# Kernel tuning notes

Hardware: AMD Instinct MI355X
Metric: run time of the kernel (lower is better)

Reference implementation:

```python
import jax, jax.numpy as jnp
import numpy as np

SAMPLING = 16   # VGG16 feature stride
POOL = 7        # adaptive max pool output size
KMAX = 5        # max bin window; valid for ROI feature extents <= 28 cells
NEG = jnp.float32(-1e30)


def _bin_bounds(s0, L, i):
    # torch AdaptiveMaxPool2d bin i over a length-L crop starting at s0:
    # [s0 + floor(i*L/P), s0 + ceil((i+1)*L/P))
    bs = s0 + (i * L) // POOL
    be = s0 + ((i + 1) * L + POOL - 1) // POOL
    return bs, be


def setup_inputs() -> dict:
    key = jax.random.key(0)
    ks = jax.random.split(key, 12)
    N, C, Hf, Wf = 1024, 512, 50, 84
    Himg, Wimg = Hf * SAMPLING, Wf * SAMPLING
    # post-ReLU VGG features -> non-negative
    featmap = jax.random.uniform(ks[0], (1, C, Hf, Wf), dtype=jnp.float32)
    # ROI boxes [x0, y0, x1, y1] in pixel coords, extents in [32, 448] px
    x0 = jax.random.randint(ks[1], (N,), 0, Wimg - 448)
    y0 = jax.random.randint(ks[2], (N,), 0, Himg - 448)
    w = jax.random.randint(ks[3], (N,), 32, 449)
    h = jax.random.randint(ks[4], (N,), 32, 449)
    roi = jnp.stack([x0, y0, x0 + w, y0 + h], axis=1).astype(jnp.int32)
    d = C * POOL * POOL  # 25088
    W1 = jax.random.normal(ks[5], (d, 4096), dtype=jnp.float32) * 0.01
    b1 = jnp.zeros((4096,), jnp.float32)
    W2 = jax.random.normal(ks[6], (4096, 4096), dtype=jnp.float32) * 0.01
    b2 = jnp.zeros((4096,), jnp.float32)
    Wc = jax.random.normal(ks[7], (4096, 3), dtype=jnp.float32) * 0.01
    bc = jnp.zeros((3,), jnp.float32)
    Wr = jax.random.normal(ks[8], (4096, 12), dtype=jnp.float32) * 0.01
    br = jnp.zeros((12,), jnp.float32)
    return {"featmap": featmap, "roi": roi, "W1": W1, "b1": b1, "W2": W2,
            "b2": b2, "Wc": Wc, "bc": bc, "Wr": Wr, "br": br}


def _roipool(featmap, roi):
    fm = featmap[0]                       # (C, Hf, Wf)
    C, Hf, Wf = fm.shape
    rf = roi // SAMPLING                  # floor, coords are non-negative
    x0, y0, x1, y1 = rf[:, 0], rf[:, 1], rf[:, 2], rf[:, 3]
    # width expand: if x1-x0 <= 1 -> grow right if in-bounds else grow left
    nw = (x1 - x0) <= 1
    x0n = jnp.where(nw & ~(x1 < Wf), x0 - 1, x0)
    x1n = jnp.where(nw & (x1 < Wf), x1 + 1, x1)
    nh = (y1 - y0) <= 1
    y0n = jnp.where(nh & ~(y1 < Hf), y0 - 1, y0)
    y1n = jnp.where(nh & (y1 < Hf), y1 + 1, y1)
    # python slice semantics clamp to array bounds
    xs, xe = jnp.clip(x0n, 0, Wf), jnp.clip(x1n, 0, Wf)
    ys, ye = jnp.clip(y0n, 0, Hf), jnp.clip(y1n, 0, Hf)
    Lx, Ly = xe - xs, ye - ys
    ar = jnp.arange(KMAX)
    rows = []
    for i in range(POOL):                 # fixed 7x7 bins
        hs, he = _bin_bounds(ys, Ly, i)
        h_idx = hs[:, None] + ar          # (N, K)
        h_ok = h_idx < he[:, None]
        h_idx = jnp.clip(h_idx, 0, Hf - 1)
        cols = []
        for j in range(POOL):
            ws_, we_ = _bin_bounds(xs, Lx, j)
            w_idx = ws_[:, None] + ar     # (N, K)
            w_ok = w_idx < we_[:, None]
            w_idx = jnp.clip(w_idx, 0, Wf - 1)
            patch = fm[:, h_idx[:, :, None], w_idx[:, None, :]]  # (C, N, K, K)
            m = h_ok[:, :, None] & w_ok[:, None, :]              # (N, K, K)
            patch = jnp.where(m[None], patch, NEG)
            cols.append(patch.max(axis=(2, 3)))                  # (C, N)
        rows.append(jnp.stack(cols, 0))   # (7, C, N)
    pool = jnp.stack(rows, 0)             # (7, 7, C, N)
    return pool.transpose(3, 2, 0, 1).reshape(roi.shape[0], -1)  # (N, C*49)


def reference(featmap, roi, W1, b1, W2, b2, Wc, bc, Wr, br):
    pooled = _roipool(featmap, roi)       # (N, 25088)
    h = (pooled @ W1 + b1) @ W2 + b2      # two Linears, no activation (as in source)
    output_cls = jax.nn.softmax(h @ Wc + bc, axis=1)
    output_reg = h @ Wr + br
    return output_cls, output_reg
```

## Files before the change

kernel.cpp:

```cpp
#include <hip/hip_runtime.h>
#include <hip/hip_bf16.h>
#include <cstdint>
#include <cstddef>

typedef __attribute__((ext_vector_type(4))) float f32x4;
typedef __attribute__((ext_vector_type(8))) short s16x8;
typedef __attribute__((ext_vector_type(4))) unsigned short u16x4;

__device__ __forceinline__ unsigned short f2bf(float f) {
    union { float f; unsigned u; } v; v.f = f;
    unsigned u = v.u;
    u += 0x7fffu + ((u >> 16) & 1u);
    return (unsigned short)(u >> 16);
}
__device__ __forceinline__ float lo_f(unsigned v) {
    union { unsigned u; float f; } w; w.u = v << 16; return w.f;
}
__device__ __forceinline__ float hi_f(unsigned v) {
    union { unsigned u; float f; } w; w.u = v & 0xffff0000u; return w.f;
}


__global__ __launch_bounds__(512) void prepA(
        const float* __restrict__ fm, unsigned short* __restrict__ fmT,
        const float* __restrict__ W2, const float* __restrict__ Wc,
        const float* __restrict__ Wr, float* __restrict__ partial1) {
    const int g5 = blockIdx.x / 5, r5 = blockIdx.x % 5;
    const int t = threadIdx.x;
    if (r5 < 4) {
        const int unit = g5 * 4 + r5;
        if (unit >= 1056) return;
        __shared__ float tile[2][32][33];
        const int sub = t >> 8, tt = t & 255;
        const int tid = unit * 2 + sub;
        const int p0 = (tid % 132) * 32, c0 = (tid / 132) * 32;
        const int tx = tt & 31, ty = tt >> 5;
        #pragma unroll
        for (int yy = ty; yy < 32; yy += 8) {
            int p = p0 + tx;
            if (p < 4200) tile[sub][yy][tx] = fm[(size_t)(c0 + yy) * 4200 + p];
        }
        __syncthreads();
        #pragma unroll
        for (int yy = ty; yy < 32; yy += 8) {
            int p = p0 + yy;
            if (p < 4200) fmT[(size_t)p * 512 + c0 + tx] = f2bf(tile[sub][tx][yy]);
        }
    } else {
        const int v = g5;
        if (v >= 256) return;
        const int bx = v & 31, ky = v >> 5;
        const int lane = t & 63, wave = t >> 6;
        const int r0 = bx * 128 + wave * 16;
        const int k0 = ky * 512;
        const int lr = lane & 15, lks = lane >> 4;
        const float* ap = W2 + (size_t)(r0 + lr) * 4096 + k0 + lks * 8;
        f32x4 acc = {0.f, 0.f, 0.f, 0.f};
        for (int s = 0; s < 16; ++s) {
            f32x4 f0 = *(const f32x4*)(ap + s * 32);
            f32x4 f1 = *(const f32x4*)(ap + s * 32 + 4);
            union { unsigned short us[8]; s16x8 v; } a, b;
            const int i0 = k0 + s * 32 + lks * 8;
            #pragma unroll
            for (int e = 0; e < 8; ++e) {
                int i = i0 + e;
                float bv = (lr < 3) ? Wc[i * 3 + lr] : (lr < 15) ? Wr[i * 12 + lr - 3] : 0.f;
                b.us[e] = f2bf(bv);
            }
            a.us[0] = f2bf(f0.x); a.us[1] = f2bf(f0.y);
            a.us[2] = f2bf(f0.z); a.us[3] = f2bf(f0.w);
            a.us[4] = f2bf(f1.x); a.us[5] = f2bf(f1.y);
            a.us[6] = f2bf(f1.z); a.us[7] = f2bf(f1.w);
            acc = __builtin_amdgcn_mfma_f32_16x16x32_bf16(a.v, b.v, acc, 0, 0, 0);
        }
        const int row = r0 + (lane >> 4) * 4;
        float* op = partial1 + ((size_t)ky * 4096 + row) * 16 + lr;
        #pragma unroll
        for (int q = 0; q < 4; ++q) op[q * 16] = acc[q];
    }
}

__global__ __launch_bounds__(256) void reduce_wf(
        const float* __restrict__ partial1, const float* __restrict__ b2,
        const float* __restrict__ Wc, const float* __restrict__ Wr,
        const float* __restrict__ bc, const float* __restrict__ br,
        float* __restrict__ Wf16, unsigned short* __restrict__ WfT,
        float* __restrict__ bfv) {
    const int t = threadIdx.x;
    if (blockIdx.x < 256) {
        int idx = blockIdx.x * 256 + t;
        float s = 0.f;
        #pragma unroll
        for (int sp = 0; sp < 8; ++sp) s += partial1[sp * 65536 + idx];
        Wf16[idx] = s;
        int i = idx >> 4, j = idx & 15;
        WfT[(size_t)j * 4096 + i] = f2bf(s);
    } else {
        float acc[15];
        #pragma unroll
        for (int j = 0; j < 15; ++j) acc[j] = 0.f;
        for (int i = t; i < 4096; i += 256) {
            float bv = b2[i];
            #pragma unroll
            for (int j = 0; j < 15; ++j)
                acc[j] += bv * ((j < 3) ? Wc[i * 3 + j] : Wr[i * 12 + (j - 3)]);
        }
        const int lane = t & 63, wv = t >> 6;
        __shared__ float red[4][15];
        #pragma unroll
        for (int j = 0; j < 15; ++j) {
            float x = acc[j];
            #pragma unroll
            for (int off = 32; off >= 1; off >>= 1) x += __shfl_xor(x, off, 64);
            if (lane == 0) red[wv][j] = x;
        }
        __syncthreads();
        if (t < 15)
            bfv[t] = red[0][t] + red[1][t] + red[2][t] + red[3][t]
                   + ((t < 3) ? bc[t] : br[t - 3]);
    }
}

#define PB(NH, NW) { \
    uint2 v[NH * NW]; \
    _Pragma("unroll") for (int r = 0; r < NH; ++r) \
        _Pragma("unroll") for (int s = 0; s < NW; ++s) \
            v[r * NW + s] = *(const uint2*)(base + ho[r] + wo[s]); \
    float a0 = lo_f(v[0].x), a1 = hi_f(v[0].x); \
    float a2 = lo_f(v[0].y), a3 = hi_f(v[0].y); \
    _Pragma("unroll") for (int q = 1; q < NH * NW; ++q) { \
        a0 = fmaxf(a0, lo_f(v[q].x)); a1 = fmaxf(a1, hi_f(v[q].x)); \
        a2 = fmaxf(a2, lo_f(v[q].y)); a3 = fmaxf(a3, hi_f(v[q].y)); } \
    m0 = a0; m1 = a1; m2 = a2; m3 = a3; } break;

__global__ __launch_bounds__(256) void megaB(
        const unsigned short* __restrict__ fmT, const int* __restrict__ roi,
        unsigned short* __restrict__ pooled,
        const float* __restrict__ W1, const unsigned short* __restrict__ WfT,
        float* __restrict__ partial2) {
    const int g4 = blockIdx.x >> 2, r4 = blockIdx.x & 3;
    const int t = threadIdx.x;
    if (r4 < 3) {
        const int sb = g4 * 3 + r4;
        if (sb >= 3136) return;
        const int bx = sb % 392, ky = sb / 392;
        const int lane = t & 63, wave = t >> 6;
        const int r0 = bx * 64 + wave * 16;
        const int k0 = ky * 512;
        const int lr = lane & 15, lks = lane >> 4;
        const float* ap = W1 + (size_t)(r0 + lr) * 4096 + k0 + lks * 8;
        const unsigned short* bp = WfT + (size_t)lr * 4096 + k0 + lks * 8;
        f32x4 acc = {0.f, 0.f, 0.f, 0.f};
        #pragma unroll 4
        for (int s = 0; s < 16; ++s) {
            f32x4 f0 = __builtin_nontemporal_load((const f32x4*)(ap + s * 32));
            f32x4 f1 = __builtin_nontemporal_load((const f32x4*)(ap + s * 32 + 4));
            s16x8 b = *(const s16x8*)(bp + s * 32);
            union { unsigned short us[8]; s16x8 v; } a;
            a.us[0] = f2bf(f0.x); a.us[1] = f2bf(f0.y);
            a.us[2] = f2bf(f0.z); a.us[3] = f2bf(f0.w);
            a.us[4] = f2bf(f1.x); a.us[5] = f2bf(f1.y);
            a.us[6] = f2bf(f1.z); a.us[7] = f2bf(f1.w);
            acc = __builtin_amdgcn_mfma_f32_16x16x32_bf16(a.v, b, acc, 0, 0, 0);
        }
        const int row = r0 + (lane >> 4) * 4;
        float* op = partial2 + ((size_t)ky * 25088 + row) * 16 + lr;
        #pragma unroll
        for (int q = 0; q < 4; ++q) __builtin_nontemporal_store(acc[q], op + q * 16);
    } else {
        const int n = g4;
        if (n >= 1024) return;
        __shared__ int hoff[7][5], woff[7][5], hcnt[7], wcnt[7];
        if (t == 0) {
            int x0 = roi[n*4+0] / 16, y0 = roi[n*4+1] / 16;
            int x1 = roi[n*4+2] / 16, y1 = roi[n*4+3] / 16;
            if (x1 - x0 <= 1) { if (x1 < 84) x1 += 1; else x0 -= 1; }
            if (y1 - y0 <= 1) { if (y1 < 50) y1 += 1; else y0 -= 1; }
            int xs = min(max(x0, 0), 84), xe = min(max(x1, 0), 84);
            int ys = min(max(y0, 0), 50), ye = min(max(y1, 0), 50);
            int Lx = xe - xs, Ly = ye - ys;
            #pragma unroll
            for (int i = 0; i < 7; ++i) {
                int b0 = ys + (i * Ly) / 7, b1 = ys + ((i + 1) * Ly + 6) / 7;
                hcnt[i] = min(b1, b0 + 5) - b0;
                int c0 = xs + (i * Lx) / 7, c1 = xs + ((i + 1) * Lx + 6) / 7;
                wcnt[i] = min(c1, c0 + 5) - c0;
                #pragma unroll
                for (int q = 0; q < 5; ++q) {
                    hoff[i][q] = (b0 + q) * 43008;
                    woff[i][q] = (c0 + q) * 512;
                }
            }
        }
        __syncthreads();
        const int g = t >> 7;
        const int c4 = (t & 127) * 4;
        const unsigned short* base = fmT + c4;
        unsigned short* orow = pooled + (size_t)n * 25088;
        for (int bp = 0; bp < 25; ++bp) {
            int bin = bp * 2 + g;
            if (bin < 49) {
                int bi = bin / 7, bj = bin - bi * 7;
                int ho[5], wo[5];
                #pragma unroll
                for (int q = 0; q < 5; ++q) { ho[q] = hoff[bi][q]; wo[q] = woff[bj][q]; }
                int nh = hcnt[bi], nw = wcnt[bj];
                float m0, m1, m2, m3;
                switch ((nh - 1) * 5 + (nw - 1)) {
                    case  0: PB(1,1)  case  1: PB(1,2)  case  2: PB(1,3)
                    case  3: PB(1,4)  case  4: PB(1,5)
                    case  5: PB(2,1)  case  6: PB(2,2)  case  7: PB(2,3)
                    case  8: PB(2,4)  case  9: PB(2,5)
                    case 10: PB(3,1)  case 11: PB(3,2)  case 12: PB(3,3)
                    case 13: PB(3,4)  case 14: PB(3,5)
                    case 15: PB(4,1)  case 16: PB(4,2)  case 17: PB(4,3)
                    case 18: PB(4,4)  case 19: PB(4,5)
                    case 20: PB(5,1)  case 21: PB(5,2)  case 22: PB(5,3)
                    case 23: PB(5,4)  case 24: PB(5,5)
                    default: m0 = m1 = m2 = m3 = 0.f; break;
                }
                u16x4 o;
                o.x = f2bf(m0); o.y = f2bf(m1); o.z = f2bf(m2); o.w = f2bf(m3);
                __builtin_nontemporal_store(o, (u16x4*)(orow + bin * 512 + c4));
            }
        }
    }
}

__global__ __launch_bounds__(256) void reduce_wbig(
        const float* __restrict__ partial2, const float* __restrict__ Wf16,
        const float* __restrict__ bfv, const float* __restrict__ b1,
        unsigned short* __restrict__ WbigT, float* __restrict__ bbig) {
    const int t = threadIdx.x;
    if (blockIdx.x < 98) {
        const int r = blockIdx.x * 256 + t;
        float sj[16];
        #pragma unroll
        for (int j = 0; j < 16; ++j) sj[j] = 0.f;
        #pragma unroll
        for (int sp = 0; sp < 8; ++sp) {
            const float4* pp = (const float4*)(partial2 + ((size_t)sp * 25088 + r) * 16);
            float4 a = pp[0], b = pp[1], c = pp[2], d = pp[3];
            sj[0] += a.x; sj[1] += a.y; sj[2]  += a.z; sj[3]  += a.w;
            sj[4] += b.x; sj[5] += b.y; sj[6]  += b.z; sj[7]  += b.w;
            sj[8] += c.x; sj[9] += c.y; sj[10] += c.z; sj[11] += c.w;
            sj[12] += d.x; sj[13] += d.y; sj[14] += d.z; sj[15] += d.w;
        }
        const int c = r / 49, bin = r - c * 49;
        const int p = bin * 512 + c;
        #pragma unroll
        for (int j = 0; j < 16; ++j)
            WbigT[(size_t)j * 25088 + p] = f2bf(sj[j]);
    } else {
        float acc[15];
        #pragma unroll
        for (int j = 0; j < 15; ++j) acc[j] = 0.f;
        for (int i = t; i < 4096; i += 256) {
            float bv = b1[i];
            #pragma unroll
            for (int j = 0; j < 15; ++j) acc[j] += bv * Wf16[i * 16 + j];
        }
        const int lane = t & 63, wv = t >> 6;
        __shared__ float red[4][15];
        #pragma unroll
        for (int j = 0; j < 15; ++j) {
            float x = acc[j];
            #pragma unroll
            for (int off = 32; off >= 1; off >>= 1) x += __shfl_xor(x, off, 64);
            if (lane == 0) red[wv][j] = x;
        }
        __syncthreads();
        if (t < 16) {
            float s = 0.f;
            if (t < 15)
                s = red[0][t] + red[1][t] + red[2][t] + red[3][t] + bfv[t];
            bbig[t] = s;
        }
    }
}

__global__ __launch_bounds__(256) void final_gemm(
        const unsigned short* __restrict__ pooled,
        const unsigned short* __restrict__ WbigT,
        float* __restrict__ partialG) {
    const int t = threadIdx.x, lane = t & 63, wave = t >> 6;
    const int m0 = blockIdx.x * 16, kz = blockIdx.y;
    const int lr = lane & 15, lks = lane >> 4;
    f32x4 acc = {0.f, 0.f, 0.f, 0.f};
    const unsigned short* arow = pooled + (size_t)(m0 + lr) * 25088 + kz * 3136 + lks * 8;
    const unsigned short* brow = WbigT + (size_t)lr * 25088 + kz * 3136 + lks * 8;
    for (int s = wave; s < 98; s += 4) {
        s16x8 a = __builtin_nontemporal_load((const s16x8*)(arow + s * 32));
        s16x8 b = *(const s16x8*)(brow + s * 32);
        acc = __builtin_amdgcn_mfma_f32_16x16x32_bf16(a, b, acc, 0, 0, 0);
    }
    __shared__ float red[4][64][4];
    #pragma unroll
    for (int r = 0; r < 4; ++r) red[wave][lane][r] = acc[r];
    __syncthreads();
    if (wave == 0) {
        #pragma unroll
        for (int r = 0; r < 4; ++r) {
            float s = red[0][lane][r] + red[1][lane][r] + red[2][lane][r] + red[3][lane][r];
            int row = m0 + (lane >> 4) * 4 + r;
            partialG[((size_t)kz * 1024 + row) * 16 + (lane & 15)] = s;
        }
    }
}

__global__ __launch_bounds__(256) void finalize_kernel(
        const float* __restrict__ partialG, const float* __restrict__ bbig,
        float* __restrict__ out) {
    const int m = blockIdx.x * 256 + threadIdx.x;
    float v[15];
    #pragma unroll
    for (int j = 0; j < 15; ++j) v[j] = bbig[j];
    for (int kz = 0; kz < 8; ++kz) {
        const float* p = partialG + ((size_t)kz * 1024 + m) * 16;
        #pragma unroll
        for (int j = 0; j < 15; ++j) v[j] += p[j];
    }
    float mx = fmaxf(v[0], fmaxf(v[1], v[2]));
    float e0 = expf(v[0] - mx), e1 = expf(v[1] - mx), e2 = expf(v[2] - mx);
    float inv = 1.f / (e0 + e1 + e2);
    out[m * 3 + 0] = e0 * inv;
    out[m * 3 + 1] = e1 * inv;
    out[m * 3 + 2] = e2 * inv;
    #pragma unroll
    for (int j = 3; j < 15; ++j) out[3072 + m * 12 + (j - 3)] = v[j];
}

extern "C" void kernel_launch(void* const* d_in, const int* in_sizes, int n_in,
                              void* d_out, int out_size, void* d_ws, size_t ws_size,
                              hipStream_t stream) {
    const float* featmap = (const float*)d_in[0];
    const int*   roi     = (const int*)d_in[1];
    const float* W1      = (const float*)d_in[2];
    const float* b1      = (const float*)d_in[3];
    const float* W2      = (const float*)d_in[4];
    const float* b2      = (const float*)d_in[5];
    const float* Wc      = (const float*)d_in[6];
    const float* bc      = (const float*)d_in[7];
    const float* Wr      = (const float*)d_in[8];
    const float* br      = (const float*)d_in[9];
    float* out = (float*)d_out;

    char* ws = (char*)d_ws;
    unsigned short* pooled   = (unsigned short*)(ws);
    unsigned short* fmT      = (unsigned short*)(ws + 51380224);
    unsigned short* WfT      = (unsigned short*)(ws + 55681024);
    float*          Wf16     = (float*)        (ws + 55812096);
    float*          bfv      = (float*)        (ws + 56074240);
    float*          bbig     = (float*)        (ws + 56074304);
    float*          partial1 = (float*)        (ws + 56074432);
    float*          partial2 = (float*)        (ws + 60268800);
    unsigned short* WbigT    = (unsigned short*)(ws + 111649024);
    float*          partialG = (float*)        (ws + 112451840);

    prepA<<<1320, 512, 0, stream>>>(featmap, fmT, W2, Wc, Wr, partial1);
    reduce_wf<<<257, 256, 0, stream>>>(partial1, b2, Wc, Wr, bc, br, Wf16, WfT, bfv);
    megaB<<<4184, 256, 0, stream>>>(fmT, roi, pooled, W1, WfT, partial2);
    reduce_wbig<<<99, 256, 0, stream>>>(partial2, Wf16, bfv, b1, WbigT, bbig);
    final_gemm<<<dim3(64, 8), 256, 0, stream>>>(pooled, WbigT, partialG);
    finalize_kernel<<<4, 256, 0, stream>>>(partialG, bbig, out);
}
```

Measured before the change: 225.5 us.

## Rebalance fused megaB: 512-thread blocks, split ROI pooling channels in halves

The fused kernel moves to 512-thread blocks. Each GEMM-part block now covers 128 rows of W1 instead of 64, so there are half as many such blocks. The ROI pooling work is split so each ROI uses two blocks, each handling half the channels with 32-bit loads (2 bf16) instead of 64-bit loads. The interleave ratio changes from 3 GEMM blocks : 1 ROI block to 14 : 18 per group of 32 blocks. The goal is to raise parallelism and memory-level concurrency for the gather-heavy pooling and to rebalance it against the streaming W1 work, at the cost of narrower loads and duplicated ROI bin setup.

```diff
diff --git a/kernel.cpp b/kernel.cpp
--- a/kernel.cpp
+++ b/kernel.cpp
@@ -5,7 +5,6 @@
 
 typedef __attribute__((ext_vector_type(4))) float f32x4;
 typedef __attribute__((ext_vector_type(8))) short s16x8;
-typedef __attribute__((ext_vector_type(4))) unsigned short u16x4;
 
 __device__ __forceinline__ unsigned short f2bf(float f) {
     union { float f; unsigned u; } v; v.f = f;
@@ -121,31 +120,29 @@
     }
 }
 
-#define PB(NH, NW) { \
-    uint2 v[NH * NW]; \
+#define PB1(NH, NW) { \
+    unsigned v[NH * NW]; \
     _Pragma("unroll") for (int r = 0; r < NH; ++r) \
         _Pragma("unroll") for (int s = 0; s < NW; ++s) \
-            v[r * NW + s] = *(const uint2*)(base + ho[r] + wo[s]); \
-    float a0 = lo_f(v[0].x), a1 = hi_f(v[0].x); \
-    float a2 = lo_f(v[0].y), a3 = hi_f(v[0].y); \
+            v[r * NW + s] = *(const unsigned*)(base + ho[r] + wo[s]); \
+    float a0 = lo_f(v[0]), a1 = hi_f(v[0]); \
     _Pragma("unroll") for (int q = 1; q < NH * NW; ++q) { \
-        a0 = fmaxf(a0, lo_f(v[q].x)); a1 = fmaxf(a1, hi_f(v[q].x)); \
-        a2 = fmaxf(a2, lo_f(v[q].y)); a3 = fmaxf(a3, hi_f(v[q].y)); } \
-    m0 = a0; m1 = a1; m2 = a2; m3 = a3; } break;
-
-__global__ __launch_bounds__(256) void megaB(
+        a0 = fmaxf(a0, lo_f(v[q])); a1 = fmaxf(a1, hi_f(v[q])); } \
+    m0 = a0; m1 = a1; } break;
+
+__global__ __launch_bounds__(512) void megaB(
         const unsigned short* __restrict__ fmT, const int* __restrict__ roi,
         unsigned short* __restrict__ pooled,
         const float* __restrict__ W1, const unsigned short* __restrict__ WfT,
         float* __restrict__ partial2) {
-    const int g4 = blockIdx.x >> 2, r4 = blockIdx.x & 3;
+    const int G = blockIdx.x >> 5, s5 = blockIdx.x & 31;
     const int t = threadIdx.x;
-    if (r4 < 3) {
-        const int sb = g4 * 3 + r4;
-        if (sb >= 3136) return;
-        const int bx = sb % 392, ky = sb / 392;
+    if (s5 < 14) {
+        const int sb = G * 14 + s5;
+        if (sb >= 1568) return;
+        const int bx = sb % 196, ky = sb / 196;
         const int lane = t & 63, wave = t >> 6;
-        const int r0 = bx * 64 + wave * 16;
+        const int r0 = bx * 128 + wave * 16;
         const int k0 = ky * 512;
         const int lr = lane & 15, lks = lane >> 4;
         const float* ap = W1 + (size_t)(r0 + lr) * 4096 + k0 + lks * 8;
@@ -168,7 +165,8 @@
         #pragma unroll
         for (int q = 0; q < 4; ++q) __builtin_nontemporal_store(acc[q], op + q * 16);
     } else {
-        const int n = g4;
+        const int h = s5 & 1;
+        const int n = G * 9 + ((s5 - 14) >> 1);
         if (n >= 1024) return;
         __shared__ int hoff[7][5], woff[7][5], hcnt[7], wcnt[7];
         if (t == 0) {
@@ -194,34 +192,33 @@
         }
         __syncthreads();
         const int g = t >> 7;
-        const int c4 = (t & 127) * 4;
-        const unsigned short* base = fmT + c4;
+        const int c2 = h * 256 + (t & 127) * 2;
+        const unsigned short* base = fmT + c2;
         unsigned short* orow = pooled + (size_t)n * 25088;
-        for (int bp = 0; bp < 25; ++bp) {
-            int bin = bp * 2 + g;
+        for (int bp = 0; bp < 13; ++bp) {
+            int bin = bp * 4 + g;
             if (bin < 49) {
                 int bi = bin / 7, bj = bin - bi * 7;
                 int ho[5], wo[5];
                 #pragma unroll
                 for (int q = 0; q < 5; ++q) { ho[q] = hoff[bi][q]; wo[q] = woff[bj][q]; }
                 int nh = hcnt[bi], nw = wcnt[bj];
-                float m0, m1, m2, m3;
+                float m0, m1;
                 switch ((nh - 1) * 5 + (nw - 1)) {
-                    case  0: PB(1,1)  case  1: PB(1,2)  case  2: PB(1,3)
-                    case  3: PB(1,4)  case  4: PB(1,5)
-                    case  5: PB(2,1)  case  6: PB(2,2)  case  7: PB(2,3)
-                    case  8: PB(2,4)  case  9: PB(2,5)
-                    case 10: PB(3,1)  case 11: PB(3,2)  case 12: PB(3,3)
-                    case 13: PB(3,4)  case 14: PB(3,5)
-                    case 15: PB(4,1)  case 16: PB(4,2)  case 17: PB(4,3)
-                    case 18: PB(4,4)  case 19: PB(4,5)
-                    case 20: PB(5,1)  case 21: PB(5,2)  case 22: PB(5,3)
-                    case 23: PB(5,4)  case 24: PB(5,5)
-                    default: m0 = m1 = m2 = m3 = 0.f; break;
+                    case  0: PB1(1,1)  case  1: PB1(1,2)  case  2: PB1(1,3)
+                    case  3: PB1(1,4)  case  4: PB1(1,5)
+                    case  5: PB1(2,1)  case  6: PB1(2,2)  case  7: PB1(2,3)
+                    case  8: PB1(2,4)  case  9: PB1(2,5)
+                    case 10: PB1(3,1)  case 11: PB1(3,2)  case 12: PB1(3,3)
+                    case 13: PB1(3,4)  case 14: PB1(3,5)
+                    case 15: PB1(4,1)  case 16: PB1(4,2)  case 17: PB1(4,3)
+                    case 18: PB1(4,4)  case 19: PB1(4,5)
+                    case 20: PB1(5,1)  case 21: PB1(5,2)  case 22: PB1(5,3)
+                    case 23: PB1(5,4)  case 24: PB1(5,5)
+                    default: m0 = m1 = 0.f; break;
                 }
-                u16x4 o;
-                o.x = f2bf(m0); o.y = f2bf(m1); o.z = f2bf(m2); o.w = f2bf(m3);
-                __builtin_nontemporal_store(o, (u16x4*)(orow + bin * 512 + c4));
+                unsigned o = (unsigned)f2bf(m0) | ((unsigned)f2bf(m1) << 16);
+                __builtin_nontemporal_store(o, (unsigned*)(orow + bin * 512 + c2));
             }
         }
     }
@@ -359,7 +356,7 @@
 
     prepA<<<1320, 512, 0, stream>>>(featmap, fmT, W2, Wc, Wr, partial1);
     reduce_wf<<<257, 256, 0, stream>>>(partial1, b2, Wc, Wr, bc, br, Wf16, WfT, bfv);
-    megaB<<<4184, 256, 0, stream>>>(fmT, roi, pooled, W1, WfT, partial2);
+    megaB<<<3648, 512, 0, stream>>>(fmT, roi, pooled, W1, WfT, partial2);
     reduce_wbig<<<99, 256, 0, stream>>>(partial2, Wf16, bfv, b1, WbigT, bbig);
     final_gemm<<<dim3(64, 8), 256, 0, stream>>>(pooled, WbigT, partialG);
     finalize_kernel<<<4, 256, 0, stream>>>(partialG, bbig, out);
```

Measured after the change: 275.8 us. 22.3% more time.

## Stage W1 tiles into LDS with async global_load_lds double buffering in megaB

Applied to the files above, without the earlier changes.

The W1 x Wf GEMM part of megaB now uses 512-thread blocks covering 128 rows by 2048 K. W1 tiles are streamed into a swizzled, double-buffered 32KB LDS area via global_load_lds, with waitcnt plus barrier per K step. This cuts the K split from 8 to 2, so reduce_wbig sums fewer partials, and it rebalances the interleaving of ROI-pool blocks (13 per group, 4 bins per pass). The goal is better latency hiding of the dominant 400MB W1 stream. The cost is two barriers per iteration and fewer blocks in flight.

```diff
diff --git a/kernel.cpp b/kernel.cpp
--- a/kernel.cpp
+++ b/kernel.cpp
@@ -18,6 +18,11 @@
 }
 __device__ __forceinline__ float hi_f(unsigned v) {
     union { unsigned u; float f; } w; w.u = v & 0xffff0000u; return w.f;
+}
+__device__ __forceinline__ void glds16(const void* g, void* l) {
+    __builtin_amdgcn_global_load_lds(
+        (const __attribute__((address_space(1))) unsigned int*)g,
+        (__attribute__((address_space(3))) unsigned int*)l, 16, 0, 0);
 }
 
 
@@ -133,42 +138,67 @@
         a2 = fmaxf(a2, lo_f(v[q].y)); a3 = fmaxf(a3, hi_f(v[q].y)); } \
     m0 = a0; m1 = a1; m2 = a2; m3 = a3; } break;
 
-__global__ __launch_bounds__(256) void megaB(
+__global__ __launch_bounds__(512) void megaB(
         const unsigned short* __restrict__ fmT, const int* __restrict__ roi,
         unsigned short* __restrict__ pooled,
         const float* __restrict__ W1, const unsigned short* __restrict__ WfT,
         float* __restrict__ partial2) {
-    const int g4 = blockIdx.x >> 2, r4 = blockIdx.x & 3;
+    __shared__ char smemA[32768];
+    const int G = blockIdx.x / 18, r18 = blockIdx.x % 18;
     const int t = threadIdx.x;
-    if (r4 < 3) {
-        const int sb = g4 * 3 + r4;
-        if (sb >= 3136) return;
-        const int bx = sb % 392, ky = sb / 392;
+    if (r18 < 5) {
+        const int sb = G * 5 + r18;
+        if (sb >= 392) return;
+        const int bx = sb % 196, ky = sb / 196;
+        const int r0 = bx * 128;
+        const int k0 = ky * 2048;
         const int lane = t & 63, wave = t >> 6;
-        const int r0 = bx * 64 + wave * 16;
-        const int k0 = ky * 512;
         const int lr = lane & 15, lks = lane >> 4;
-        const float* ap = W1 + (size_t)(r0 + lr) * 4096 + k0 + lks * 8;
-        const unsigned short* bp = WfT + (size_t)lr * 4096 + k0 + lks * 8;
+
+        auto STAGE = [&](int th) {
+            if (th >= 64) return;
+            char* lbase = smemA + (th & 1) * 16384;
+            #pragma unroll
+            for (int ci = 0; ci < 2; ++ci) {
+                int S = ci * 512 + t;
+                int row = S >> 3, cs = S & 7;
+                int csw = cs ^ (row & 7);
+                glds16(W1 + (size_t)(r0 + row) * 4096 + k0 + th * 32 + csw * 4,
+                       lbase + S * 16);
+            }
+        };
+        STAGE(0);
         f32x4 acc = {0.f, 0.f, 0.f, 0.f};
-        #pragma unroll 4
-        for (int s = 0; s < 16; ++s) {
-            f32x4 f0 = __builtin_nontemporal_load((const f32x4*)(ap + s * 32));
-            f32x4 f1 = __builtin_nontemporal_load((const f32x4*)(ap + s * 32 + 4));
-            s16x8 b = *(const s16x8*)(bp + s * 32);
+        const unsigned short* bbase = WfT + (size_t)lr * 4096 + k0 + lks * 8;
+        const int row = wave * 16 + lr;
+        const int g0 = lks * 2;
+        const int offA = (row * 8 + (g0 ^ (row & 7))) * 16;
+        const int offB = (row * 8 + ((g0 + 1) ^ (row & 7))) * 16;
+        for (int th = 0; th < 64; ++th) {
+            s16x8 bfrag = *(const s16x8*)(bbase + th * 32);
+            STAGE(th + 1);
+            if (th == 63) asm volatile("s_waitcnt vmcnt(0)" ::: "memory");
+            else          asm volatile("s_waitcnt vmcnt(2)" ::: "memory");
+            __builtin_amdgcn_s_barrier();
+            asm volatile("" ::: "memory");
+            const char* buf = smemA + (th & 1) * 16384;
+            f32x4 fa = *(const f32x4*)(buf + offA);
+            f32x4 fb = *(const f32x4*)(buf + offB);
             union { unsigned short us[8]; s16x8 v; } a;
-            a.us[0] = f2bf(f0.x); a.us[1] = f2bf(f0.y);
-            a.us[2] = f2bf(f0.z); a.us[3] = f2bf(f0.w);
-            a.us[4] = f2bf(f1.x); a.us[5] = f2bf(f1.y);
-            a.us[6] = f2bf(f1.z); a.us[7] = f2bf(f1.w);
-            acc = __builtin_amdgcn_mfma_f32_16x16x32_bf16(a.v, b, acc, 0, 0, 0);
-        }
-        const int row = r0 + (lane >> 4) * 4;
-        float* op = partial2 + ((size_t)ky * 25088 + row) * 16 + lr;
+            a.us[0] = f2bf(fa.x); a.us[1] = f2bf(fa.y);
+            a.us[2] = f2bf(fa.z); a.us[3] = f2bf(fa.w);
+            a.us[4] = f2bf(fb.x); a.us[5] = f2bf(fb.y);
+            a.us[6] = f2bf(fb.z); a.us[7] = f2bf(fb.w);
+            acc = __builtin_amdgcn_mfma_f32_16x16x32_bf16(a.v, bfrag, acc, 0, 0, 0);
+            asm volatile("" ::: "memory");
+            __builtin_amdgcn_s_barrier();
+        }
+        const int orow = r0 + wave * 16 + lks * 4;
+        float* op = partial2 + ((size_t)ky * 25088 + orow) * 16 + lr;
         #pragma unroll
         for (int q = 0; q < 4; ++q) __builtin_nontemporal_store(acc[q], op + q * 16);
     } else {
-        const int n = g4;
+        const int n = G * 13 + (r18 - 5);
         if (n >= 1024) return;
         __shared__ int hoff[7][5], woff[7][5], hcnt[7], wcnt[7];
         if (t == 0) {
@@ -197,8 +227,8 @@
         const int c4 = (t & 127) * 4;
         const unsigned short* base = fmT + c4;
         unsigned short* orow = pooled + (size_t)n * 25088;
-        for (int bp = 0; bp < 25; ++bp) {
-            int bin = bp * 2 + g;
+        for (int bp = 0; bp < 13; ++bp) {
+            int bin = bp * 4 + g;
             if (bin < 49) {
                 int bi = bin / 7, bj = bin - bi * 7;
                 int ho[5], wo[5];
@@ -238,7 +268,7 @@
         #pragma unroll
         for (int j = 0; j < 16; ++j) sj[j] = 0.f;
         #pragma unroll
-        for (int sp = 0; sp < 8; ++sp) {
+        for (int sp = 0; sp < 2; ++sp) {
             const float4* pp = (const float4*)(partial2 + ((size_t)sp * 25088 + r) * 16);
             float4 a = pp[0], b = pp[1], c = pp[2], d = pp[3];
             sj[0] += a.x; sj[1] += a.y; sj[2]  += a.z; sj[3]  += a.w;
@@ -359,7 +389,7 @@
 
     prepA<<<1320, 512, 0, stream>>>(featmap, fmT, W2, Wc, Wr, partial1);
     reduce_wf<<<257, 256, 0, stream>>>(partial1, b2, Wc, Wr, bc, br, Wf16, WfT, bfv);
-    megaB<<<4184, 256, 0, stream>>>(fmT, roi, pooled, W1, WfT, partial2);
+    megaB<<<1422, 512, 0, stream>>>(fmT, roi, pooled, W1, WfT, partial2);
     reduce_wbig<<<99, 256, 0, stream>>>(partial2, Wf16, bfv, b1, WbigT, bbig);
     final_gemm<<<dim3(64, 8), 256, 0, stream>>>(pooled, WbigT, partialG);
     finalize_kernel<<<4, 256, 0, stream>>>(partialG, bbig, out);
```

New measurement: 259.8 us. 1.15x slower.
